# Kernel optimization log

Hardware: AMD Instinct MI355X
Metric: run time of the kernel (lower is better)

The kernel has to match this reference:

```python
import jax, jax.numpy as jnp
import numpy as np

NBINS = 256       # kornia equalize_clahe default histogram bins
GRID = (8, 8)     # kornia default grid_size


def _clahe(x, clip_limit):
    """kornia-style CLAHE on x:(C,H,W) in [0,1]; H,W divisible by GRID."""
    C, H, W = x.shape
    GH, GW = GRID
    TH, TW = H // GH, W // GW
    pixels = TH * TW
    # ---- per-tile histograms via flat scatter-add (irregular core) ----
    b_hist = jnp.clip((x * NBINS).astype(jnp.int32), 0, NBINS - 1)  # torch.histc(min=0,max=1) bins
    tiles = b_hist.reshape(C, GH, TH, GW, TW).transpose(0, 1, 3, 2, 4).reshape(-1, pixels)
    ntiles = tiles.shape[0]  # C*GH*GW
    flat = (tiles + (jnp.arange(ntiles, dtype=jnp.int32) * NBINS)[:, None]).ravel()
    hist = jnp.zeros((ntiles * NBINS,), x.dtype).at[flat].add(1.0).reshape(ntiles, NBINS)
    # ---- clip and redistribute excess (kornia _compute_luts) ----
    max_val = jnp.maximum(jnp.floor(clip_limit * pixels / NBINS), 1.0)
    clipped = jnp.minimum(hist, max_val)
    excess = pixels - clipped.sum(-1)                    # (ntiles,), >= 0
    residual = jnp.mod(excess, NBINS)
    redist = (excess - residual) / NBINS
    hist = clipped + redist[:, None] + (jnp.arange(NBINS) < residual[:, None]).astype(x.dtype)
    # ---- LUT from CDF ----
    lut = jnp.floor(jnp.clip(jnp.cumsum(hist, -1) * (NBINS - 1) / pixels, 0, NBINS - 1))
    lut = lut.reshape(C, GH, GW, NBINS)
    # ---- per-pixel bilinear interpolation between 4 neighbouring tile LUTs ----
    def coords(n, T, G):
        g = (jnp.arange(n) + 0.5) / T - 0.5    # fractional tile coordinate
        lo = jnp.clip(jnp.floor(g), 0, G - 1).astype(jnp.int32)
        hi = jnp.clip(lo + 1, 0, G - 1)
        w = jnp.clip(g - jnp.floor(g), 0.0, 1.0).astype(x.dtype)
        return lo, hi, w
    y0, y1, wy = coords(H, TH, GH)
    x0, x1, wx = coords(W, TW, GW)
    b = jnp.clip(jnp.floor(x * (NBINS - 1)).astype(jnp.int32), 0, NBINS - 1)  # lookup bin
    c = jnp.arange(C)[:, None, None]
    def g(ty, tx):  # gather lut[c, ty[h], tx[w], b[c,h,w]] -> (C,H,W)
        return lut[c, ty[None, :, None], tx[None, None, :], b]
    top = g(y0, x0) * (1 - wx)[None, None, :] + g(y0, x1) * wx[None, None, :]
    bot = g(y1, x0) * (1 - wx)[None, None, :] + g(y1, x1) * wx[None, None, :]
    out = top * (1 - wy)[None, :, None] + bot * wy[None, :, None]
    return out / (NBINS - 1)


def _forward(x, log_cor=True):
    shape = x.shape
    mean = x.mean()
    std = jnp.std(x, ddof=1)            # torch .std() is unbiased
    x = (x - mean) / std                # TF.normalize
    xmin, xmax = x.min(), x.max()
    x = (x - xmin) / (xmax - xmin)      # normalize_in_range(x, 0, 1)
    ct_proxy = jnp.std(x, ddof=1)       # x.std([0,1,2]) on 3D input = scalar
    def clahe_branch(xx):
        beta = 10.0 * ct_proxy
        cl = 1.0 / (1.0 - beta) + beta  # data-dependent clip limit
        return _clahe(xx, cl)
    x = jax.lax.cond(ct_proxy < 0.05, clahe_branch, lambda xx: xx, x)
    if log_cor:
        x = jnp.log2(1.0 + x)           # adjust_log with gain=1
    return x.reshape(shape)


def setup_inputs() -> dict:
    key = jax.random.key(0)
    x = jax.random.normal(key, (32, 1024, 1024), dtype=jnp.float32)
    # heavy-tailed distribution -> std/range (ct_proxy) ~ 0.01 < 0.05 so CLAHE branch runs
    x = x ** 3
    return {"x": x}


def reference(x):
    return _forward(x, log_cor=True)
```

## Files before the change

### kernel.cpp

```cpp
#include <hip/hip_runtime.h>
#include <math.h>

#define NC 32
#define NH 1024
#define NW 1024
#define NTH 128
#define NTW 128
#define NBINS 256
#define NTILES (NC*8*8)
#define NPIXTOT (NC*NH*NW)
#define TPIX (NTH*NTW)

#define OFF_PSUM   0
#define OFF_PSQ    16384
#define OFF_PMIN   32768
#define OFF_PMAX   40960
#define OFF_PARAMS 49152
#define OFF_LUT8   65536

__global__ __launch_bounds__(256) void k_reduce(const float* __restrict__ x,
                                                double* __restrict__ ps,
                                                double* __restrict__ ps2,
                                                float* __restrict__ pmn,
                                                float* __restrict__ pmx) {
    int tid = threadIdx.x;
    long g = (long)blockIdx.x * 256 + tid;
    double sa = 0.0, sb = 0.0, s2a = 0.0, s2b = 0.0;
    float mn = INFINITY, mx = -INFINITY;
    const float4* x4 = (const float4*)x;
    const long n4 = NPIXTOT / 4;
    const long stride = (long)2048 * 256;
    for (long i = g; i < n4; i += 2 * stride) {
        float4 v = x4[i];
        float sf  = (v.x + v.y) + (v.z + v.w);
        float s2f = fmaf(v.x, v.x, fmaf(v.y, v.y, fmaf(v.z, v.z, v.w * v.w)));
        sa  += (double)sf;
        s2a += (double)s2f;
        mn = fminf(mn, fminf(fminf(v.x, v.y), fminf(v.z, v.w)));
        mx = fmaxf(mx, fmaxf(fmaxf(v.x, v.y), fmaxf(v.z, v.w)));
        long i2 = i + stride;
        if (i2 < n4) {
            float4 u = x4[i2];
            float sg  = (u.x + u.y) + (u.z + u.w);
            float s2g = fmaf(u.x, u.x, fmaf(u.y, u.y, fmaf(u.z, u.z, u.w * u.w)));
            sb  += (double)sg;
            s2b += (double)s2g;
            mn = fminf(mn, fminf(fminf(u.x, u.y), fminf(u.z, u.w)));
            mx = fmaxf(mx, fmaxf(fmaxf(u.x, u.y), fmaxf(u.z, u.w)));
        }
    }
    double s = sa + sb, s2 = s2a + s2b;
    for (int o = 32; o; o >>= 1) {
        s  += __shfl_down(s, o);
        s2 += __shfl_down(s2, o);
        mn = fminf(mn, __shfl_down(mn, o));
        mx = fmaxf(mx, __shfl_down(mx, o));
    }
    __shared__ double shs[4], shs2[4];
    __shared__ float shmn[4], shmx[4];
    int wid = tid >> 6, lane = tid & 63;
    if (lane == 0) { shs[wid] = s; shs2[wid] = s2; shmn[wid] = mn; shmx[wid] = mx; }
    __syncthreads();
    if (tid == 0) {
        double S  = shs[0] + shs[1] + shs[2] + shs[3];
        double S2 = shs2[0] + shs2[1] + shs2[2] + shs2[3];
        float MN = fminf(fminf(shmn[0], shmn[1]), fminf(shmn[2], shmn[3]));
        float MX = fmaxf(fmaxf(shmx[0], shmx[1]), fmaxf(shmx[2], shmx[3]));
        ps[blockIdx.x] = S; ps2[blockIdx.x] = S2; pmn[blockIdx.x] = MN; pmx[blockIdx.x] = MX;
    }
}

__global__ __launch_bounds__(256) void k_histlut(const float* __restrict__ x,
                                                 const double* __restrict__ ps,
                                                 const double* __restrict__ ps2,
                                                 const float* __restrict__ pmn,
                                                 const float* __restrict__ pmx,
                                                 float* __restrict__ params,
                                                 unsigned char* __restrict__ lut8) {
    __shared__ unsigned lh[4 * NBINS];
    __shared__ int sh[NBINS];
    __shared__ double shs[4], shs2[4];
    __shared__ float shmn[4], shmx[4], spar[4];
    int tid = threadIdx.x;
    int t = blockIdx.x;
    int lane = tid & 63;
    int wid = tid >> 6;

    double s = 0.0, s2 = 0.0;
    float mn = INFINITY, mx = -INFINITY;
    for (int i = tid; i < 2048; i += 256) {
        s += ps[i]; s2 += ps2[i];
        mn = fminf(mn, pmn[i]); mx = fmaxf(mx, pmx[i]);
    }
    for (int o = 32; o; o >>= 1) {
        s  += __shfl_down(s, o);
        s2 += __shfl_down(s2, o);
        mn = fminf(mn, __shfl_down(mn, o));
        mx = fmaxf(mx, __shfl_down(mx, o));
    }
    if (lane == 0) { shs[wid] = s; shs2[wid] = s2; shmn[wid] = mn; shmx[wid] = mx; }
    __syncthreads();
    if (tid == 0) {
        double S  = shs[0] + shs[1] + shs[2] + shs[3];
        double S2 = shs2[0] + shs2[1] + shs2[2] + shs2[3];
        float MN = fminf(fminf(shmn[0], shmn[1]), fminf(shmn[2], shmn[3]));
        float MX = fmaxf(fmaxf(shmx[0], shmx[1]), fmaxf(shmx[2], shmx[3]));
        const double n = (double)NPIXTOT;
        double var = (S2 - S * S / n) / (n - 1.0);
        double sd = sqrt(var > 0.0 ? var : 0.0);
        double range = (double)MX - (double)MN;
        double ct = sd / range;
        int flag = (ct < 0.05) ? 1 : 0;
        double beta = 10.0 * ct;
        double cl = 1.0 / (1.0 - beta) + beta;
        double mv = floor(cl * (double)TPIX / (double)NBINS);
        if (mv < 1.0) mv = 1.0;
        spar[0] = MN;
        spar[1] = (float)(1.0 / range);
        spar[2] = (float)mv;
        if (t == 0) {
            params[0] = MN;
            params[1] = (float)(1.0 / range);
            params[2] = (float)mv;
            ((int*)params)[3] = flag;
        }
    }
    #pragma unroll
    for (int w = 0; w < 4; w++) lh[w * NBINS + tid] = 0;
    __syncthreads();
    float xmin = spar[0], inv = spar[1];
    int mv = (int)spar[2];

    int c = t >> 6, gy = (t >> 3) & 7, gx = t & 7;
    const float* base = x + ((long)c * NH + (long)gy * NTH) * NW + gx * NTW;
    unsigned* mylh = lh + wid * NBINS;
    #pragma unroll 4
    for (int j = 0; j < 16; j++) {
        int l = j * 256 + tid;
        int th = l >> 5, tw4 = l & 31;
        float4 v = *(const float4*)(base + (long)th * NW + tw4 * 4);
        float z0 = (v.x - xmin) * inv;
        float z1 = (v.y - xmin) * inv;
        float z2 = (v.z - xmin) * inv;
        float z3 = (v.w - xmin) * inv;
        int b0 = (int)(z0 * 256.0f); b0 = b0 < 0 ? 0 : (b0 > 255 ? 255 : b0);
        int b1 = (int)(z1 * 256.0f); b1 = b1 < 0 ? 0 : (b1 > 255 ? 255 : b1);
        int b2 = (int)(z2 * 256.0f); b2 = b2 < 0 ? 0 : (b2 > 255 ? 255 : b2);
        int b3 = (int)(z3 * 256.0f); b3 = b3 < 0 ? 0 : (b3 > 255 ? 255 : b3);
        int d = __builtin_amdgcn_readfirstlane(b0);
        int cnt = (b0 == d) + (b1 == d) + (b2 == d) + (b3 == d);
        #pragma unroll
        for (int m = 1; m < 64; m <<= 1) cnt += __shfl_xor(cnt, m);
        if (lane == 0 && cnt > 0) atomicAdd(&mylh[d], (unsigned)cnt);
        if (b0 != d) atomicAdd(&mylh[b0], 1u);
        if (b1 != d) atomicAdd(&mylh[b1], 1u);
        if (b2 != d) atomicAdd(&mylh[b2], 1u);
        if (b3 != d) atomicAdd(&mylh[b3], 1u);
    }
    __syncthreads();

    int h = (int)(lh[tid] + lh[NBINS + tid] + lh[2 * NBINS + tid] + lh[3 * NBINS + tid]);
    int cl = h < mv ? h : mv;
    sh[tid] = cl;
    __syncthreads();
    for (int o = 1; o < NBINS; o <<= 1) {
        int v = (tid >= o) ? sh[tid - o] : 0;
        __syncthreads();
        sh[tid] += v;
        __syncthreads();
    }
    int total = sh[NBINS - 1];
    int cdfc = sh[tid];
    int excess = TPIX - total;
    int residual = excess & (NBINS - 1);
    int redist = excess >> 8;
    int cdf = cdfc + redist * (tid + 1) + ((tid + 1) < residual ? (tid + 1) : residual);
    float lv = floorf(fminf((float)cdf * 255.0f / 16384.0f, 255.0f));
    int iv = (int)(lv < 0.0f ? 0.0f : lv);
    lut8[t * NBINS + tid] = (unsigned char)iv;
}

__global__ __launch_bounds__(256) void k_out(const float* __restrict__ x,
                                             const float* __restrict__ params,
                                             const unsigned char* __restrict__ lut8,
                                             float* __restrict__ out) {
    __shared__ unsigned char slut[4096];
    int tid = threadIdx.x;
    int r = blockIdx.x;
    int c = r >> 10;
    int h = r & (NH - 1);
    float xmin = params[0], inv = params[1];
    int flag = ((const int*)params)[3];
    float gy = (h + 0.5f) * (1.0f / NTH) - 0.5f;
    float fy = floorf(gy);
    float wy = gy - fy;
    int y0 = (int)fy; y0 = y0 < 0 ? 0 : (y0 > 7 ? 7 : y0);
    int y1 = y0 + 1 > 7 ? 7 : y0 + 1;
    const unsigned char* src0 = lut8 + ((long)c * 64 + y0 * 8) * NBINS;
    const unsigned char* src1 = lut8 + ((long)c * 64 + y1 * 8) * NBINS;
    if (tid < 128) {
        *(uint4*)(slut + tid * 16) = *(const uint4*)(src0 + tid * 16);
    } else {
        int u = tid - 128;
        *(uint4*)(slut + 2048 + u * 16) = *(const uint4*)(src1 + u * 16);
    }
    __syncthreads();
    long p = ((long)r << 10) + tid * 4;
    float4 v = *(const float4*)(x + p);
    float zv[4] = {v.x, v.y, v.z, v.w};
    float o4[4];
    #pragma unroll
    for (int k = 0; k < 4; k++) {
        float z = (zv[k] - xmin) * inv;
        float val;
        if (flag) {
            int wk = tid * 4 + k;
            float gxc = (wk + 0.5f) * (1.0f / NTW) - 0.5f;
            float fx = floorf(gxc);
            float wx = gxc - fx;
            int x0 = (int)fx; x0 = x0 < 0 ? 0 : (x0 > 7 ? 7 : x0);
            int x1 = x0 + 1 > 7 ? 7 : x0 + 1;
            int b = (int)(z * 255.0f);
            b = b < 0 ? 0 : (b > 255 ? 255 : b);
            float l00 = (float)slut[x0 * NBINS + b];
            float l01 = (float)slut[x1 * NBINS + b];
            float l10 = (float)slut[2048 + x0 * NBINS + b];
            float l11 = (float)slut[2048 + x1 * NBINS + b];
            float top = l00 * (1.0f - wx) + l01 * wx;
            float bot = l10 * (1.0f - wx) + l11 * wx;
            val = (top * (1.0f - wy) + bot * wy) * (1.0f / 255.0f);
        } else {
            val = z;
        }
        o4[k] = log2f(1.0f + val);
    }
    *(float4*)(out + p) = make_float4(o4[0], o4[1], o4[2], o4[3]);
}

extern "C" void kernel_launch(void* const* d_in, const int* in_sizes, int n_in,
                              void* d_out, int out_size, void* d_ws, size_t ws_size,
                              hipStream_t stream) {
    const float* x = (const float*)d_in[0];
    float* out = (float*)d_out;
    char* ws = (char*)d_ws;
    double* ps   = (double*)(ws + OFF_PSUM);
    double* ps2  = (double*)(ws + OFF_PSQ);
    float* pmn   = (float*)(ws + OFF_PMIN);
    float* pmx   = (float*)(ws + OFF_PMAX);
    float* params= (float*)(ws + OFF_PARAMS);
    unsigned char* lut8 = (unsigned char*)(ws + OFF_LUT8);

    k_reduce<<<2048, 256, 0, stream>>>(x, ps, ps2, pmn, pmx);
    k_histlut<<<NTILES, 256, 0, stream>>>(x, ps, ps2, pmn, pmx, params, lut8);
    k_out<<<NC * NH, 256, 0, stream>>>(x, params, lut8, out);
}
```

Baseline: 304.1 us.

## Fuse reduce, histogram/LUT and output into one cooperative persistent kernel

Replaces the three kernel launches with a single cooperative kernel of 1024 blocks that uses grid-wide syncs between the global stats reduction, per-tile histogram/LUT build (two tiles per block), and the output pass. Each block then processes 32 rows of output and reloads the tile-row LUTs into shared memory only when the tile row changes. This aims to remove launch gaps and the repeated per-row LUT staging. In exchange it adds grid-sync cost, fixes occupancy to what co-residency allows, and each block runs its histogram tiles serially.

```diff
diff --git a/kernel.cpp b/kernel.cpp
--- a/kernel.cpp
+++ b/kernel.cpp
@@ -1,5 +1,8 @@
 #include <hip/hip_runtime.h>
+#include <hip/hip_cooperative_groups.h>
 #include <math.h>
+
+namespace cg = cooperative_groups;
 
 #define NC 32
 #define NH 1024
@@ -7,234 +10,227 @@
 #define NTH 128
 #define NTW 128
 #define NBINS 256
-#define NTILES (NC*8*8)
-#define NPIXTOT (NC*NH*NW)
-#define TPIX (NTH*NTW)
-
-#define OFF_PSUM   0
-#define OFF_PSQ    16384
-#define OFF_PMIN   32768
-#define OFF_PMAX   40960
-#define OFF_PARAMS 49152
-#define OFF_LUT8   65536
-
-__global__ __launch_bounds__(256) void k_reduce(const float* __restrict__ x,
-                                                double* __restrict__ ps,
-                                                double* __restrict__ ps2,
-                                                float* __restrict__ pmn,
-                                                float* __restrict__ pmx) {
-    int tid = threadIdx.x;
-    long g = (long)blockIdx.x * 256 + tid;
-    double sa = 0.0, sb = 0.0, s2a = 0.0, s2b = 0.0;
-    float mn = INFINITY, mx = -INFINITY;
-    const float4* x4 = (const float4*)x;
-    const long n4 = NPIXTOT / 4;
-    const long stride = (long)2048 * 256;
-    for (long i = g; i < n4; i += 2 * stride) {
-        float4 v = x4[i];
-        float sf  = (v.x + v.y) + (v.z + v.w);
-        float s2f = fmaf(v.x, v.x, fmaf(v.y, v.y, fmaf(v.z, v.z, v.w * v.w)));
-        sa  += (double)sf;
-        s2a += (double)s2f;
-        mn = fminf(mn, fminf(fminf(v.x, v.y), fminf(v.z, v.w)));
-        mx = fmaxf(mx, fmaxf(fmaxf(v.x, v.y), fmaxf(v.z, v.w)));
-        long i2 = i + stride;
-        if (i2 < n4) {
-            float4 u = x4[i2];
+#define NTILES 2048
+#define NPIXTOT 33554432
+#define TPIX 16384
+#define NBLK 1024
+
+#define OFF_PSUM 0
+#define OFF_PSQ  8192
+#define OFF_PMIN 16384
+#define OFF_PMAX 20480
+#define OFF_LUT8 24576
+
+__global__ __launch_bounds__(256, 4) void k_mega(
+    const float* __restrict__ x,
+    double* __restrict__ ps, double* __restrict__ ps2,
+    float* __restrict__ pmn, float* __restrict__ pmx,
+    unsigned char* __restrict__ lut8,
+    float* __restrict__ out)
+{
+    cg::grid_group grid = cg::this_grid();
+    const int tid = threadIdx.x;
+    const int bid = blockIdx.x;
+    const int lane = tid & 63, wid = tid >> 6;
+
+    __shared__ double shs[4], shs2[4];
+    __shared__ float shmn[4], shmx[4];
+    __shared__ float spar[3];
+    __shared__ int sflag;
+    __shared__ unsigned lh[4 * NBINS];
+    __shared__ int sh[NBINS];
+    __shared__ unsigned char slut[4096];
+
+    {
+        long g = (long)bid * 256 + tid;
+        double sa = 0.0, sb = 0.0, s2a = 0.0, s2b = 0.0;
+        float mn = INFINITY, mx = -INFINITY;
+        const float4* x4 = (const float4*)x;
+        const long stride = (long)NBLK * 256;
+        for (long i = g; i < (long)(NPIXTOT / 4); i += 2 * stride) {
+            float4 v = x4[i];
+            float4 u = x4[i + stride];
+            float sf  = (v.x + v.y) + (v.z + v.w);
+            float s2f = fmaf(v.x, v.x, fmaf(v.y, v.y, fmaf(v.z, v.z, v.w * v.w)));
             float sg  = (u.x + u.y) + (u.z + u.w);
             float s2g = fmaf(u.x, u.x, fmaf(u.y, u.y, fmaf(u.z, u.z, u.w * u.w)));
-            sb  += (double)sg;
-            s2b += (double)s2g;
+            sa += (double)sf;  s2a += (double)s2f;
+            sb += (double)sg;  s2b += (double)s2g;
+            mn = fminf(mn, fminf(fminf(v.x, v.y), fminf(v.z, v.w)));
+            mx = fmaxf(mx, fmaxf(fmaxf(v.x, v.y), fmaxf(v.z, v.w)));
             mn = fminf(mn, fminf(fminf(u.x, u.y), fminf(u.z, u.w)));
             mx = fmaxf(mx, fmaxf(fmaxf(u.x, u.y), fmaxf(u.z, u.w)));
         }
-    }
-    double s = sa + sb, s2 = s2a + s2b;
-    for (int o = 32; o; o >>= 1) {
-        s  += __shfl_down(s, o);
-        s2 += __shfl_down(s2, o);
-        mn = fminf(mn, __shfl_down(mn, o));
-        mx = fmaxf(mx, __shfl_down(mx, o));
-    }
-    __shared__ double shs[4], shs2[4];
-    __shared__ float shmn[4], shmx[4];
-    int wid = tid >> 6, lane = tid & 63;
-    if (lane == 0) { shs[wid] = s; shs2[wid] = s2; shmn[wid] = mn; shmx[wid] = mx; }
-    __syncthreads();
-    if (tid == 0) {
-        double S  = shs[0] + shs[1] + shs[2] + shs[3];
-        double S2 = shs2[0] + shs2[1] + shs2[2] + shs2[3];
-        float MN = fminf(fminf(shmn[0], shmn[1]), fminf(shmn[2], shmn[3]));
-        float MX = fmaxf(fmaxf(shmx[0], shmx[1]), fmaxf(shmx[2], shmx[3]));
-        ps[blockIdx.x] = S; ps2[blockIdx.x] = S2; pmn[blockIdx.x] = MN; pmx[blockIdx.x] = MX;
-    }
-}
-
-__global__ __launch_bounds__(256) void k_histlut(const float* __restrict__ x,
-                                                 const double* __restrict__ ps,
-                                                 const double* __restrict__ ps2,
-                                                 const float* __restrict__ pmn,
-                                                 const float* __restrict__ pmx,
-                                                 float* __restrict__ params,
-                                                 unsigned char* __restrict__ lut8) {
-    __shared__ unsigned lh[4 * NBINS];
-    __shared__ int sh[NBINS];
-    __shared__ double shs[4], shs2[4];
-    __shared__ float shmn[4], shmx[4], spar[4];
-    int tid = threadIdx.x;
-    int t = blockIdx.x;
-    int lane = tid & 63;
-    int wid = tid >> 6;
-
-    double s = 0.0, s2 = 0.0;
-    float mn = INFINITY, mx = -INFINITY;
-    for (int i = tid; i < 2048; i += 256) {
-        s += ps[i]; s2 += ps2[i];
-        mn = fminf(mn, pmn[i]); mx = fmaxf(mx, pmx[i]);
-    }
-    for (int o = 32; o; o >>= 1) {
-        s  += __shfl_down(s, o);
-        s2 += __shfl_down(s2, o);
-        mn = fminf(mn, __shfl_down(mn, o));
-        mx = fmaxf(mx, __shfl_down(mx, o));
-    }
-    if (lane == 0) { shs[wid] = s; shs2[wid] = s2; shmn[wid] = mn; shmx[wid] = mx; }
-    __syncthreads();
-    if (tid == 0) {
-        double S  = shs[0] + shs[1] + shs[2] + shs[3];
-        double S2 = shs2[0] + shs2[1] + shs2[2] + shs2[3];
-        float MN = fminf(fminf(shmn[0], shmn[1]), fminf(shmn[2], shmn[3]));
-        float MX = fmaxf(fmaxf(shmx[0], shmx[1]), fmaxf(shmx[2], shmx[3]));
-        const double n = (double)NPIXTOT;
-        double var = (S2 - S * S / n) / (n - 1.0);
-        double sd = sqrt(var > 0.0 ? var : 0.0);
-        double range = (double)MX - (double)MN;
-        double ct = sd / range;
-        int flag = (ct < 0.05) ? 1 : 0;
-        double beta = 10.0 * ct;
-        double cl = 1.0 / (1.0 - beta) + beta;
-        double mv = floor(cl * (double)TPIX / (double)NBINS);
-        if (mv < 1.0) mv = 1.0;
-        spar[0] = MN;
-        spar[1] = (float)(1.0 / range);
-        spar[2] = (float)mv;
-        if (t == 0) {
-            params[0] = MN;
-            params[1] = (float)(1.0 / range);
-            params[2] = (float)mv;
-            ((int*)params)[3] = flag;
-        }
-    }
-    #pragma unroll
-    for (int w = 0; w < 4; w++) lh[w * NBINS + tid] = 0;
-    __syncthreads();
-    float xmin = spar[0], inv = spar[1];
-    int mv = (int)spar[2];
-
-    int c = t >> 6, gy = (t >> 3) & 7, gx = t & 7;
-    const float* base = x + ((long)c * NH + (long)gy * NTH) * NW + gx * NTW;
-    unsigned* mylh = lh + wid * NBINS;
-    #pragma unroll 4
-    for (int j = 0; j < 16; j++) {
-        int l = j * 256 + tid;
-        int th = l >> 5, tw4 = l & 31;
-        float4 v = *(const float4*)(base + (long)th * NW + tw4 * 4);
-        float z0 = (v.x - xmin) * inv;
-        float z1 = (v.y - xmin) * inv;
-        float z2 = (v.z - xmin) * inv;
-        float z3 = (v.w - xmin) * inv;
-        int b0 = (int)(z0 * 256.0f); b0 = b0 < 0 ? 0 : (b0 > 255 ? 255 : b0);
-        int b1 = (int)(z1 * 256.0f); b1 = b1 < 0 ? 0 : (b1 > 255 ? 255 : b1);
-        int b2 = (int)(z2 * 256.0f); b2 = b2 < 0 ? 0 : (b2 > 255 ? 255 : b2);
-        int b3 = (int)(z3 * 256.0f); b3 = b3 < 0 ? 0 : (b3 > 255 ? 255 : b3);
-        int d = __builtin_amdgcn_readfirstlane(b0);
-        int cnt = (b0 == d) + (b1 == d) + (b2 == d) + (b3 == d);
+        double s = sa + sb, s2 = s2a + s2b;
+        for (int o = 32; o; o >>= 1) {
+            s  += __shfl_down(s, o);
+            s2 += __shfl_down(s2, o);
+            mn = fminf(mn, __shfl_down(mn, o));
+            mx = fmaxf(mx, __shfl_down(mx, o));
+        }
+        if (lane == 0) { shs[wid] = s; shs2[wid] = s2; shmn[wid] = mn; shmx[wid] = mx; }
+        __syncthreads();
+        if (tid == 0) {
+            ps[bid]  = shs[0] + shs[1] + shs[2] + shs[3];
+            ps2[bid] = shs2[0] + shs2[1] + shs2[2] + shs2[3];
+            pmn[bid] = fminf(fminf(shmn[0], shmn[1]), fminf(shmn[2], shmn[3]));
+            pmx[bid] = fmaxf(fmaxf(shmx[0], shmx[1]), fmaxf(shmx[2], shmx[3]));
+        }
+        __threadfence();
+    }
+    grid.sync();
+
+    float xmin, inv;
+    int mv, flag;
+    {
+        double s = 0.0, s2 = 0.0;
+        float mn = INFINITY, mx = -INFINITY;
+        for (int i = tid; i < NBLK; i += 256) {
+            s += ps[i]; s2 += ps2[i];
+            mn = fminf(mn, pmn[i]); mx = fmaxf(mx, pmx[i]);
+        }
+        for (int o = 32; o; o >>= 1) {
+            s  += __shfl_down(s, o);
+            s2 += __shfl_down(s2, o);
+            mn = fminf(mn, __shfl_down(mn, o));
+            mx = fmaxf(mx, __shfl_down(mx, o));
+        }
+        if (lane == 0) { shs[wid] = s; shs2[wid] = s2; shmn[wid] = mn; shmx[wid] = mx; }
+        __syncthreads();
+        if (tid == 0) {
+            double S  = shs[0] + shs[1] + shs[2] + shs[3];
+            double S2 = shs2[0] + shs2[1] + shs2[2] + shs2[3];
+            float MN = fminf(fminf(shmn[0], shmn[1]), fminf(shmn[2], shmn[3]));
+            float MX = fmaxf(fmaxf(shmx[0], shmx[1]), fmaxf(shmx[2], shmx[3]));
+            const double n = (double)NPIXTOT;
+            double var = (S2 - S * S / n) / (n - 1.0);
+            double sd = sqrt(var > 0.0 ? var : 0.0);
+            double range = (double)MX - (double)MN;
+            double ct = sd / range;
+            double beta = 10.0 * ct;
+            double cl = 1.0 / (1.0 - beta) + beta;
+            double mvd = floor(cl * (double)TPIX / (double)NBINS);
+            if (mvd < 1.0) mvd = 1.0;
+            spar[0] = MN;
+            spar[1] = (float)(1.0 / range);
+            spar[2] = (float)mvd;
+            sflag = (ct < 0.05) ? 1 : 0;
+        }
+        __syncthreads();
+        xmin = spar[0]; inv = spar[1]; mv = (int)spar[2]; flag = sflag;
+    }
+    for (int tt = 0; tt < 2; tt++) {
+        int t = bid * 2 + tt;
+        __syncthreads();
         #pragma unroll
-        for (int m = 1; m < 64; m <<= 1) cnt += __shfl_xor(cnt, m);
-        if (lane == 0 && cnt > 0) atomicAdd(&mylh[d], (unsigned)cnt);
-        if (b0 != d) atomicAdd(&mylh[b0], 1u);
-        if (b1 != d) atomicAdd(&mylh[b1], 1u);
-        if (b2 != d) atomicAdd(&mylh[b2], 1u);
-        if (b3 != d) atomicAdd(&mylh[b3], 1u);
-    }
-    __syncthreads();
-
-    int h = (int)(lh[tid] + lh[NBINS + tid] + lh[2 * NBINS + tid] + lh[3 * NBINS + tid]);
-    int cl = h < mv ? h : mv;
-    sh[tid] = cl;
-    __syncthreads();
-    for (int o = 1; o < NBINS; o <<= 1) {
-        int v = (tid >= o) ? sh[tid - o] : 0;
-        __syncthreads();
-        sh[tid] += v;
-        __syncthreads();
-    }
-    int total = sh[NBINS - 1];
-    int cdfc = sh[tid];
-    int excess = TPIX - total;
-    int residual = excess & (NBINS - 1);
-    int redist = excess >> 8;
-    int cdf = cdfc + redist * (tid + 1) + ((tid + 1) < residual ? (tid + 1) : residual);
-    float lv = floorf(fminf((float)cdf * 255.0f / 16384.0f, 255.0f));
-    int iv = (int)(lv < 0.0f ? 0.0f : lv);
-    lut8[t * NBINS + tid] = (unsigned char)iv;
-}
-
-__global__ __launch_bounds__(256) void k_out(const float* __restrict__ x,
-                                             const float* __restrict__ params,
-                                             const unsigned char* __restrict__ lut8,
-                                             float* __restrict__ out) {
-    __shared__ unsigned char slut[4096];
-    int tid = threadIdx.x;
-    int r = blockIdx.x;
-    int c = r >> 10;
-    int h = r & (NH - 1);
-    float xmin = params[0], inv = params[1];
-    int flag = ((const int*)params)[3];
-    float gy = (h + 0.5f) * (1.0f / NTH) - 0.5f;
-    float fy = floorf(gy);
-    float wy = gy - fy;
-    int y0 = (int)fy; y0 = y0 < 0 ? 0 : (y0 > 7 ? 7 : y0);
-    int y1 = y0 + 1 > 7 ? 7 : y0 + 1;
-    const unsigned char* src0 = lut8 + ((long)c * 64 + y0 * 8) * NBINS;
-    const unsigned char* src1 = lut8 + ((long)c * 64 + y1 * 8) * NBINS;
-    if (tid < 128) {
-        *(uint4*)(slut + tid * 16) = *(const uint4*)(src0 + tid * 16);
-    } else {
-        int u = tid - 128;
-        *(uint4*)(slut + 2048 + u * 16) = *(const uint4*)(src1 + u * 16);
-    }
-    __syncthreads();
-    long p = ((long)r << 10) + tid * 4;
-    float4 v = *(const float4*)(x + p);
-    float zv[4] = {v.x, v.y, v.z, v.w};
-    float o4[4];
-    #pragma unroll
-    for (int k = 0; k < 4; k++) {
-        float z = (zv[k] - xmin) * inv;
-        float val;
-        if (flag) {
-            int wk = tid * 4 + k;
-            float gxc = (wk + 0.5f) * (1.0f / NTW) - 0.5f;
-            float fx = floorf(gxc);
-            float wx = gxc - fx;
-            int x0 = (int)fx; x0 = x0 < 0 ? 0 : (x0 > 7 ? 7 : x0);
-            int x1 = x0 + 1 > 7 ? 7 : x0 + 1;
-            int b = (int)(z * 255.0f);
-            b = b < 0 ? 0 : (b > 255 ? 255 : b);
-            float l00 = (float)slut[x0 * NBINS + b];
-            float l01 = (float)slut[x1 * NBINS + b];
-            float l10 = (float)slut[2048 + x0 * NBINS + b];
-            float l11 = (float)slut[2048 + x1 * NBINS + b];
-            float top = l00 * (1.0f - wx) + l01 * wx;
-            float bot = l10 * (1.0f - wx) + l11 * wx;
-            val = (top * (1.0f - wy) + bot * wy) * (1.0f / 255.0f);
-        } else {
-            val = z;
-        }
-        o4[k] = log2f(1.0f + val);
-    }
-    *(float4*)(out + p) = make_float4(o4[0], o4[1], o4[2], o4[3]);
+        for (int w = 0; w < 4; w++) lh[w * NBINS + tid] = 0;
+        __syncthreads();
+        int c = t >> 6, gy = (t >> 3) & 7, gx = t & 7;
+        const float* base = x + ((long)c * NH + (long)gy * NTH) * NW + gx * NTW;
+        unsigned* mylh = lh + wid * NBINS;
+        #pragma unroll 4
+        for (int j = 0; j < 16; j++) {
+            int l = j * 256 + tid;
+            int th = l >> 5, tw4 = l & 31;
+            float4 v = *(const float4*)(base + (long)th * NW + tw4 * 4);
+            float z0 = (v.x - xmin) * inv;
+            float z1 = (v.y - xmin) * inv;
+            float z2 = (v.z - xmin) * inv;
+            float z3 = (v.w - xmin) * inv;
+            int b0 = (int)(z0 * 256.0f); b0 = b0 < 0 ? 0 : (b0 > 255 ? 255 : b0);
+            int b1 = (int)(z1 * 256.0f); b1 = b1 < 0 ? 0 : (b1 > 255 ? 255 : b1);
+            int b2 = (int)(z2 * 256.0f); b2 = b2 < 0 ? 0 : (b2 > 255 ? 255 : b2);
+            int b3 = (int)(z3 * 256.0f); b3 = b3 < 0 ? 0 : (b3 > 255 ? 255 : b3);
+            int d = __builtin_amdgcn_readfirstlane(b0);
+            int cnt = (b0 == d) + (b1 == d) + (b2 == d) + (b3 == d);
+            #pragma unroll
+            for (int m = 1; m < 64; m <<= 1) cnt += __shfl_xor(cnt, m);
+            if (lane == 0 && cnt > 0) atomicAdd(&mylh[d], (unsigned)cnt);
+            if (b0 != d) atomicAdd(&mylh[b0], 1u);
+            if (b1 != d) atomicAdd(&mylh[b1], 1u);
+            if (b2 != d) atomicAdd(&mylh[b2], 1u);
+            if (b3 != d) atomicAdd(&mylh[b3], 1u);
+        }
+        __syncthreads();
+        int hh = (int)(lh[tid] + lh[NBINS + tid] + lh[2 * NBINS + tid] + lh[3 * NBINS + tid]);
+        int clp = hh < mv ? hh : mv;
+        sh[tid] = clp;
+        __syncthreads();
+        for (int o = 1; o < NBINS; o <<= 1) {
+            int v = (tid >= o) ? sh[tid - o] : 0;
+            __syncthreads();
+            sh[tid] += v;
+            __syncthreads();
+        }
+        int total = sh[NBINS - 1];
+        int cdfc = sh[tid];
+        int excess = TPIX - total;
+        int residual = excess & (NBINS - 1);
+        int redist = excess >> 8;
+        int cdf = cdfc + redist * (tid + 1) + ((tid + 1) < residual ? (tid + 1) : residual);
+        float lv = floorf(fminf((float)cdf * 255.0f / 16384.0f, 255.0f));
+        int iv = (int)(lv < 0.0f ? 0.0f : lv);
+        lut8[t * NBINS + tid] = (unsigned char)iv;
+    }
+    __threadfence();
+    grid.sync();
+
+    {
+        int c = bid >> 5;
+        int h0 = (bid & 31) << 5;
+        int cy0 = -1;
+        for (int rr = 0; rr < 32; rr++) {
+            int h = h0 + rr;
+            float gyf = (h + 0.5f) * (1.0f / NTH) - 0.5f;
+            float fy = floorf(gyf);
+            float wy = gyf - fy;
+            int y0 = (int)fy; y0 = y0 < 0 ? 0 : (y0 > 7 ? 7 : y0);
+            int y1 = y0 + 1 > 7 ? 7 : y0 + 1;
+            if (y0 != cy0) {
+                __syncthreads();
+                const unsigned char* src0 = lut8 + ((long)c * 64 + y0 * 8) * NBINS;
+                const unsigned char* src1 = lut8 + ((long)c * 64 + y1 * 8) * NBINS;
+                if (tid < 128) {
+                    *(uint4*)(slut + tid * 16) = *(const uint4*)(src0 + tid * 16);
+                } else {
+                    int u2 = tid - 128;
+                    *(uint4*)(slut + 2048 + u2 * 16) = *(const uint4*)(src1 + u2 * 16);
+                }
+                __syncthreads();
+                cy0 = y0;
+            }
+            long p = ((long)c << 20) + ((long)h << 10) + tid * 4;
+            float4 v = *(const float4*)(x + p);
+            float zv[4] = {v.x, v.y, v.z, v.w};
+            float o4[4];
+            #pragma unroll
+            for (int k = 0; k < 4; k++) {
+                float z = (zv[k] - xmin) * inv;
+                float val;
+                if (flag) {
+                    int wk = tid * 4 + k;
+                    float gxc = (wk + 0.5f) * (1.0f / NTW) - 0.5f;
+                    float fx = floorf(gxc);
+                    float wx = gxc - fx;
+                    int x0 = (int)fx; x0 = x0 < 0 ? 0 : (x0 > 7 ? 7 : x0);
+                    int x1 = x0 + 1 > 7 ? 7 : x0 + 1;
+                    int b = (int)(z * 255.0f);
+                    b = b < 0 ? 0 : (b > 255 ? 255 : b);
+                    float l00 = (float)slut[x0 * NBINS + b];
+                    float l01 = (float)slut[x1 * NBINS + b];
+                    float l10 = (float)slut[2048 + x0 * NBINS + b];
+                    float l11 = (float)slut[2048 + x1 * NBINS + b];
+                    float top = l00 * (1.0f - wx) + l01 * wx;
+                    float bot = l10 * (1.0f - wx) + l11 * wx;
+                    val = (top * (1.0f - wy) + bot * wy) * (1.0f / 255.0f);
+                } else {
+                    val = z;
+                }
+                o4[k] = log2f(1.0f + val);
+            }
+            *(float4*)(out + p) = make_float4(o4[0], o4[1], o4[2], o4[3]);
+        }
+    }
 }
 
 extern "C" void kernel_launch(void* const* d_in, const int* in_sizes, int n_in,
@@ -247,10 +243,10 @@
     double* ps2  = (double*)(ws + OFF_PSQ);
     float* pmn   = (float*)(ws + OFF_PMIN);
     float* pmx   = (float*)(ws + OFF_PMAX);
-    float* params= (float*)(ws + OFF_PARAMS);
     unsigned char* lut8 = (unsigned char*)(ws + OFF_LUT8);
 
-    k_reduce<<<2048, 256, 0, stream>>>(x, ps, ps2, pmn, pmx);
-    k_histlut<<<NTILES, 256, 0, stream>>>(x, ps, ps2, pmn, pmx, params, lut8);
-    k_out<<<NC * NH, 256, 0, stream>>>(x, params, lut8, out);
+    void* args[] = { (void*)&x, (void*)&ps, (void*)&ps2, (void*)&pmn,
+                     (void*)&pmx, (void*)&lut8, (void*)&out };
+    hipLaunchCooperativeKernel((const void*)k_mega, dim3(NBLK), dim3(256),
+                               args, 0, stream);
 }
```

After: 664.8 us. 119% more time.
